# Performance work log

Measured on AMD Instinct MI355X. Metric: run time of the kernel, lower is better.

## Reference

```python
import jax, jax.numpy as jnp
import numpy as np

SEQ_LEN = 2048
NUM_HEADS = 16
DIM_EMB = 1024
DIM_HEAD = DIM_EMB // NUM_HEADS  # 64
DIM_K = DIM_EMB  # source scales by dim_k**-0.5 with dim_k defaulting to dim_emb
BASE = 10000
EPS = float(np.finfo(np.float32).eps)


def _rope_tables(seq_len, dim_head):
    idx = jnp.arange(seq_len, dtype=jnp.float32)
    scale = 1.0 / (BASE ** (jnp.arange(0, dim_head, 2, dtype=jnp.float32) / dim_head) + EPS)
    pos = jnp.outer(idx, scale)              # [S, dh/2]
    pos = jnp.concatenate([pos, pos], axis=-1)  # [S, dh]
    return jnp.cos(pos), jnp.sin(pos)


def _rotate_half(x):
    x1, x2 = x[..., : DIM_HEAD // 2], x[..., DIM_HEAD // 2 :]
    return jnp.concatenate([-x2, x1], axis=-1)


def _apply_rope(x, cos, sin):
    # x: [B, H, S, dh]; cos/sin: [S, dh]
    return x * cos[None, None] + _rotate_half(x) * sin[None, None]


def setup_inputs() -> dict:
    key = jax.random.key(0)
    k1, k2, k3 = jax.random.split(key, 3)
    x = jax.random.normal(k1, (2, SEQ_LEN, DIM_EMB), dtype=jnp.float32)
    Wqkv = jax.random.normal(k2, (DIM_EMB, 3 * DIM_EMB), dtype=jnp.float32) * 0.02
    Wout = jax.random.normal(k3, (DIM_EMB, DIM_EMB), dtype=jnp.float32) * 0.02
    return {"x": x, "Wqkv": Wqkv, "Wout": Wout}


def reference(x, Wqkv, Wout):
    B = x.shape[0]
    cos, sin = _rope_tables(SEQ_LEN, DIM_HEAD)
    qkv = x @ Wqkv  # [B, S, 3*E]
    q, k, v = jnp.split(qkv, 3, axis=-1)

    def to_heads(t):
        return t.reshape(B, SEQ_LEN, NUM_HEADS, DIM_HEAD).transpose(0, 2, 1, 3)

    q, k, v = to_heads(q), to_heads(k), to_heads(v)
    q = _apply_rope(q, cos, sin)
    k = _apply_rope(k, cos, sin)

    scores = jnp.einsum('bhsd,bhtd->bhst', q, k) * (DIM_K ** -0.5)
    causal_mask = jnp.triu(jnp.ones((SEQ_LEN, SEQ_LEN), dtype=bool), k=1)
    scores = jnp.where(causal_mask[None, None], -jnp.inf, scores)
    attn = jax.nn.softmax(scores, axis=-1)
    out = jnp.einsum('bhst,bhtd->bhsd', attn, v)
    out = out.transpose(0, 2, 1, 3).reshape(B, SEQ_LEN, DIM_EMB)
    return out @ Wout
```

## Files before the change

### kernel.cpp

```cpp
#include <hip/hip_runtime.h>

#define S_LEN 2048
#define NHEAD 16

using f32x4  = __attribute__((ext_vector_type(4))) float;
using f32x16 = __attribute__((ext_vector_type(16))) float;
using bf16x8 = __attribute__((ext_vector_type(8))) __bf16;

__device__ __forceinline__ unsigned short f2bf(float f) {
  union { float f; unsigned u; } v; v.f = f;
  unsigned r = v.u + 0x7FFFu + ((v.u >> 16) & 1u);
  return (unsigned short)(r >> 16);
}
__device__ __forceinline__ float bf2f(unsigned short h) {
  union { unsigned u; float f; } v; v.u = ((unsigned)h) << 16; return v.f;
}
__device__ __forceinline__ void unpack8(uint4 u, float x[8]) {
  x[0]=bf2f((unsigned short)(u.x&0xffff)); x[1]=bf2f((unsigned short)(u.x>>16));
  x[2]=bf2f((unsigned short)(u.y&0xffff)); x[3]=bf2f((unsigned short)(u.y>>16));
  x[4]=bf2f((unsigned short)(u.z&0xffff)); x[5]=bf2f((unsigned short)(u.z>>16));
  x[6]=bf2f((unsigned short)(u.w&0xffff)); x[7]=bf2f((unsigned short)(u.w>>16));
}
__device__ __forceinline__ uint4 pack8(const unsigned short o[8]) {
  uint4 u;
  u.x = (unsigned)o[0] | ((unsigned)o[1]<<16);
  u.y = (unsigned)o[2] | ((unsigned)o[3]<<16);
  u.z = (unsigned)o[4] | ((unsigned)o[5]<<16);
  u.w = (unsigned)o[6] | ((unsigned)o[7]<<16);
  return u;
}
__device__ __forceinline__ void gload16(const void* g, void* l) {
  __builtin_amdgcn_global_load_lds(
      (const __attribute__((address_space(1))) unsigned int*)g,
      (__attribute__((address_space(3))) unsigned int*)l, 16, 0, 0);
}
__device__ __forceinline__ float exp2_fast(float x) {
#if __has_builtin(__builtin_amdgcn_exp2f)
  return __builtin_amdgcn_exp2f(x);
#else
  return __expf(x * 0.6931471805599453f);
#endif
}
__device__ __forceinline__ void store_c(float* C, size_t off, float v) { C[off] = v; }
__device__ __forceinline__ void store_c(unsigned short* C, size_t off, float v) { C[off] = f2bf(v); }

__global__ __launch_bounds__(256) void k_cvt(const float* __restrict__ in,
                                             unsigned short* __restrict__ out, int n8) {
  int i = blockIdx.x * 256 + threadIdx.x;
  if (i >= n8) return;
  const float4* p = (const float4*)in + 2 * (size_t)i;
  float4 a = p[0], b = p[1];
  unsigned short o[8] = { f2bf(a.x), f2bf(a.y), f2bf(a.z), f2bf(a.w),
                          f2bf(b.x), f2bf(b.y), f2bf(b.z), f2bf(b.w) };
  ((uint4*)out)[i] = pack8(o);
}

__global__ __launch_bounds__(256) void k_transpose_cvt(const float* __restrict__ in,
                                                       unsigned short* __restrict__ out,
                                                       int R, int C) {
  __shared__ float T[64][65];
  int r0 = blockIdx.x * 64, c0 = blockIdx.y * 64;
  int tid = threadIdx.x;
#pragma unroll
  for (int i = 0; i < 16; ++i) {
    int idx = tid + i * 256;
    int r = idx >> 6, c = idx & 63;
    T[r][c] = in[(size_t)(r0 + r) * C + c0 + c];
  }
  __syncthreads();
#pragma unroll
  for (int i = 0; i < 8; ++i) {
    int idx = tid + i * 256;
    int co = idx >> 5, rp = (idx & 31) * 2;
    unsigned v = (unsigned)f2bf(T[rp][co]) | ((unsigned)f2bf(T[rp + 1][co]) << 16);
    *(unsigned*)&out[(size_t)(c0 + co) * R + r0 + rp] = v;
  }
}

template <typename OUT_T>
__global__ __launch_bounds__(256) void k_gemm_bt(const unsigned short* __restrict__ A,
                                                 const unsigned short* __restrict__ Bt,
                                                 OUT_T* __restrict__ C,
                                                 int M, int N, int K) {
  __shared__ unsigned short As[128 * 32];
  __shared__ unsigned short Bs[128 * 32];
  int m0 = blockIdx.x * 128, n0 = blockIdx.y * 128;
  int tid = threadIdx.x;
  int lane = tid & 63, w = tid >> 6;
  int wr = w >> 1, wc = w & 1;
  int li = lane & 15, g = lane >> 4;

  const unsigned short* a_s0 = A + (size_t)(m0 + (tid >> 2)) * K + (tid & 3) * 8;
  const unsigned short* a_s1 = A + (size_t)(m0 + 64 + (tid >> 2)) * K + (tid & 3) * 8;
  const unsigned short* b_s0 = Bt + (size_t)(n0 + (tid >> 2)) * K + (tid & 3) * 8;
  const unsigned short* b_s1 = Bt + (size_t)(n0 + 64 + (tid >> 2)) * K + (tid & 3) * 8;
  unsigned short* As_d0 = &As[(w * 64) * 8];
  unsigned short* As_d1 = &As[(256 + w * 64) * 8];
  unsigned short* Bs_d0 = &Bs[(w * 64) * 8];
  unsigned short* Bs_d1 = &Bs[(256 + w * 64) * 8];

  f32x4 acc[4][4];
#pragma unroll
  for (int i = 0; i < 4; ++i)
#pragma unroll
    for (int j = 0; j < 4; ++j) acc[i][j] = (f32x4){0.f, 0.f, 0.f, 0.f};

  int nk = K >> 5;
  for (int kt = 0; kt < nk; ++kt) {
    int k0 = kt << 5;
    gload16(a_s0 + k0, As_d0);
    gload16(a_s1 + k0, As_d1);
    gload16(b_s0 + k0, Bs_d0);
    gload16(b_s1 + k0, Bs_d1);
    __syncthreads();
    bf16x8 af[4], bfr[4];
#pragma unroll
    for (int i = 0; i < 4; ++i)
      af[i] = *(const bf16x8*)&As[(wr * 64 + i * 16 + li) * 32 + g * 8];
#pragma unroll
    for (int j = 0; j < 4; ++j)
      bfr[j] = *(const bf16x8*)&Bs[(wc * 64 + j * 16 + li) * 32 + g * 8];
#pragma unroll
    for (int i = 0; i < 4; ++i)
#pragma unroll
      for (int j = 0; j < 4; ++j)
        acc[i][j] = __builtin_amdgcn_mfma_f32_16x16x32_bf16(af[i], bfr[j], acc[i][j], 0, 0, 0);
    __syncthreads();
  }
#pragma unroll
  for (int i = 0; i < 4; ++i) {
    int row = m0 + wr * 64 + i * 16 + g * 4;
#pragma unroll
    for (int j = 0; j < 4; ++j) {
      int col = n0 + wc * 64 + j * 16 + li;
#pragma unroll
      for (int r = 0; r < 4; ++r) store_c(C, (size_t)(row + r) * N + col, acc[i][j][r]);
    }
  }
}

__global__ __launch_bounds__(512, 2) void k_gemm8(const unsigned short* __restrict__ A,
                                                  const unsigned short* __restrict__ Bt,
                                                  unsigned short* __restrict__ C,
                                                  int M, int N, int K) {
  __shared__ unsigned short As[2][256][64];
  __shared__ unsigned short Bs[2][256][64];
  const int tid = threadIdx.x;
  const int lane = tid & 63, w = tid >> 6;
  const int wm = w >> 2, wn = w & 3;
  const int li = lane & 15, g = lane >> 4;
  const int m0 = blockIdx.x * 256, n0 = blockIdx.y * 256;
  const int srow = w * 8 + (lane >> 3);
  const int scol = ((lane & 7) ^ ((lane >> 3) & 7)) * 8;

  f32x4 acc[8][4];
#pragma unroll
  for (int i = 0; i < 8; ++i)
#pragma unroll
    for (int j = 0; j < 4; ++j) acc[i][j] = (f32x4){0.f, 0.f, 0.f, 0.f};

  const int nt = K >> 6;

  auto stage_tile = [&](int kt) {
    int buf = kt & 1;
    const unsigned short* sa = A + (size_t)(m0 + srow) * K + kt * 64 + scol;
    const unsigned short* sb = Bt + (size_t)(n0 + srow) * K + kt * 64 + scol;
    char* da = (char*)&As[buf][0][0] + w * 1024;
    char* db = (char*)&Bs[buf][0][0] + w * 1024;
    gload16(sa, da);
    gload16(sa + (size_t)64 * K, da + 8192);
    gload16(sa + (size_t)128 * K, da + 16384);
    gload16(sa + (size_t)192 * K, da + 24576);
    gload16(sb, db);
    gload16(sb + (size_t)64 * K, db + 8192);
    gload16(sb + (size_t)128 * K, db + 16384);
    gload16(sb + (size_t)192 * K, db + 24576);
  };

  stage_tile(0);

  for (int i = 0; i < nt; ++i) {
    if (i + 1 < nt) {
      stage_tile(i + 1);
      asm volatile("s_waitcnt vmcnt(8)" ::: "memory");
    } else {
      asm volatile("s_waitcnt vmcnt(0)" ::: "memory");
    }
    __builtin_amdgcn_s_barrier();
    asm volatile("" ::: "memory");
    const int buf = i & 1;
#pragma unroll
    for (int kk = 0; kk < 2; ++kk) {
      bf16x8 af[8], bfv[4];
      const int ps = ((kk << 2) | g) ^ (li & 7);
#pragma unroll
      for (int ii = 0; ii < 8; ++ii)
        af[ii] = *(const bf16x8*)&As[buf][wm * 128 + ii * 16 + li][ps * 8];
#pragma unroll
      for (int jj = 0; jj < 4; ++jj)
        bfv[jj] = *(const bf16x8*)&Bs[buf][wn * 64 + jj * 16 + li][ps * 8];
      __builtin_amdgcn_s_setprio(1);
#pragma unroll
      for (int ii = 0; ii < 8; ++ii)
#pragma unroll
        for (int jj = 0; jj < 4; ++jj)
          acc[ii][jj] = __builtin_amdgcn_mfma_f32_16x16x32_bf16(af[ii], bfv[jj],
                                                                acc[ii][jj], 0, 0, 0);
      __builtin_amdgcn_s_setprio(0);
    }
    asm volatile("" ::: "memory");
    __builtin_amdgcn_s_barrier();
    asm volatile("" ::: "memory");
  }

#pragma unroll
  for (int ii = 0; ii < 8; ++ii) {
    int row = m0 + wm * 128 + ii * 16 + g * 4;
#pragma unroll
    for (int jj = 0; jj < 4; ++jj) {
      int col = n0 + wn * 64 + jj * 16 + li;
#pragma unroll
      for (int r = 0; r < 4; ++r) C[(size_t)(row + r) * N + col] = f2bf(acc[ii][jj][r]);
    }
  }
}

__global__ __launch_bounds__(256) void k_rope_split(const unsigned short* __restrict__ qkv,
                                                    unsigned short* __restrict__ Qf,
                                                    unsigned short* __restrict__ Kf,
                                                    unsigned short* __restrict__ Vf) {
  int blk = blockIdx.x;
  int st = blk & 31, h = (blk >> 5) & 15, b = blk >> 9;
  int s0 = st * 64;
  int tid = threadIdx.x;
  int sl = tid >> 2, quad = tid & 3;
  int s = s0 + sl;
  int bh = b * NHEAD + h;
  int l31 = s & 31;
  int qt = s >> 5;
  int cq = quad >> 1, hiq = quad & 1;

  float cs[8], sn[8];
#pragma unroll
  for (int j = 0; j < 8; ++j) {
    int pr = quad * 8 + j;
    float e2 = exp2_fast((float)pr * 0.41524101f);
    float freq = 1.0f / (e2 + 1.1920928955078125e-07f);
    float x = (float)s * freq * 0.15915494309189535f;
    x -= floorf(x);
    float ang = x * 6.283185307179586f;
    sn[j] = __sinf(ang);
    cs[j] = __cosf(ang);
  }
  const unsigned short* row = qkv + (size_t)(b * S_LEN + s) * 3072;
  const float QSC = 0.04508422f;
  {
    float x1[8], x2[8];
    unpack8(*(const uint4*)&row[h * 64 + quad * 8], x1);
    unpack8(*(const uint4*)&row[h * 64 + 32 + quad * 8], x2);
    unsigned short o1[8], o2[8];
#pragma unroll
    for (int j = 0; j < 8; ++j) {
      o1[j] = f2bf((x1[j] * cs[j] - x2[j] * sn[j]) * QSC);
      o2[j] = f2bf((x2[j] * cs[j] + x1[j] * sn[j]) * QSC);
    }
    size_t base = ((size_t)bh * 64 + qt) * 4;
    int lane8 = (hiq * 32 + l31) * 8;
    *(uint4*)&Qf[(base + cq) * 512 + lane8] = pack8(o1);
    *(uint4*)&Qf[(base + 2 + cq) * 512 + lane8] = pack8(o2);
  }
  {
    float x1[8], x2[8];
    unpack8(*(const uint4*)&row[1024 + h * 64 + quad * 8], x1);
    unpack8(*(const uint4*)&row[1024 + h * 64 + 32 + quad * 8], x2);
    unsigned short o1[8], o2[8];
#pragma unroll
    for (int j = 0; j < 8; ++j) {
      o1[j] = f2bf(x1[j] * cs[j] - x2[j] * sn[j]);
      o2[j] = f2bf(x2[j] * cs[j] + x1[j] * sn[j]);
    }
    int lp = (l31 & 0x13) | ((l31 & 4) << 1) | ((l31 & 8) >> 1);
    size_t base = ((size_t)bh * 64 + qt) * 4;
    int lane8 = (hiq * 32 + lp) * 8;
    *(uint4*)&Kf[(base + cq) * 512 + lane8] = pack8(o1);
    *(uint4*)&Kf[(base + 2 + cq) * 512 + lane8] = pack8(o2);
  }
  __shared__ unsigned short Vl[64 * 72];
#pragma unroll
  for (int i = 0; i < 2; ++i) {
    int c = tid + i * 256;
    int r = c >> 3, c8 = (c & 7) * 8;
    *(uint4*)&Vl[r * 72 + c8] =
        *(const uint4*)&qkv[(size_t)(b * S_LEN + s0 + r) * 3072 + 2048 + h * 64 + c8];
  }
  __syncthreads();
  int d = tid >> 2, sc4 = tid & 3;
  unsigned o[8];
#pragma unroll
  for (int jj = 0; jj < 8; ++jj) {
    int sidx = sc4 * 16 + jj * 2;
    o[jj] = (unsigned)Vl[sidx * 72 + d] | ((unsigned)Vl[(sidx + 1) * 72 + d] << 16);
  }
  {
    int t = st * 2 + (sc4 >> 1);
    int c = ((d >> 5) << 1) + (sc4 & 1);
    size_t base = (((size_t)bh * 64 + t) * 4 + c) * 512;
    *(uint4*)&Vf[base + (d & 31) * 8]        = make_uint4(o[0], o[1], o[2], o[3]);
    *(uint4*)&Vf[base + (32 + (d & 31)) * 8] = make_uint4(o[4], o[5], o[6], o[7]);
  }
}

__global__ __launch_bounds__(256) void k_attn4(const unsigned short* __restrict__ Qf,
                                               const unsigned short* __restrict__ Kf,
                                               const unsigned short* __restrict__ Vf,
                                               unsigned short* __restrict__ O) {
  __shared__ float MBUF[3][2176];
  int bid = blockIdx.x;
  int i = (bid & 7) * 256 + (bid >> 3);
  int bh = i >> 6;
  int qt = 63 - (i & 63);
  int tid = threadIdx.x, w = tid >> 6, lane = tid & 63;
  int b = bh >> 4, h = bh & 15;
  int l31 = lane & 31, hi = lane >> 5;

  int n = qt + 1;
  int t0 = (w * n) >> 2, t1 = ((w + 1) * n) >> 2;

  const unsigned short* Kg = Kf + ((size_t)bh * 64) * 4 * 512 + lane * 8;
  const unsigned short* Vg = Vf + ((size_t)bh * 64) * 4 * 512 + lane * 8;

  float m_run = -1e30f, l_run = 0.f;
  f32x16 acc0, acc1;
#pragma unroll
  for (int r = 0; r < 16; ++r) { acc0[r] = 0.f; acc1[r] = 0.f; }

  if (t0 < t1) {
    const unsigned short* Qg = Qf + (((size_t)bh * 64 + qt) * 4) * 512 + lane * 8;
    bf16x8 qf[4];
#pragma unroll
    for (int c = 0; c < 4; ++c) qf[c] = *(const bf16x8*)(Qg + c * 512);

    auto loadK = [&](bf16x8 (&kf)[4], int t) {
      const unsigned short* kp = Kg + (size_t)t * 2048;
#pragma unroll
      for (int c = 0; c < 4; ++c) kf[c] = *(const bf16x8*)(kp + c * 512);
    };
    auto loadV = [&](bf16x8 (&vf)[4], int t) {
      const unsigned short* vp = Vg + (size_t)t * 2048;
#pragma unroll
      for (int c = 0; c < 4; ++c) vf[c] = *(const bf16x8*)(vp + c * 512);
    };
    auto step = [&](bf16x8 (&kf)[4], bf16x8 (&vf)[4], int t) {
      f32x16 s;
#pragma unroll
      for (int r = 0; r < 16; ++r) s[r] = 0.f;
      __builtin_amdgcn_s_setprio(1);
      s = __builtin_amdgcn_mfma_f32_32x32x16_bf16(kf[0], qf[0], s, 0, 0, 0);
      s = __builtin_amdgcn_mfma_f32_32x32x16_bf16(kf[1], qf[1], s, 0, 0, 0);
      s = __builtin_amdgcn_mfma_f32_32x32x16_bf16(kf[2], qf[2], s, 0, 0, 0);
      s = __builtin_amdgcn_mfma_f32_32x32x16_bf16(kf[3], qf[3], s, 0, 0, 0);
      __builtin_amdgcn_s_setprio(0);
      if (t == qt) {
#pragma unroll
        for (int r = 0; r < 16; ++r) {
          int kv = (r & 7) + 16 * (r >> 3) + 8 * hi;
          if (kv > l31) s[r] = -1e30f;
        }
      }
      float pmax;
      {
        float m0 = fmaxf(s[0], s[1]),   mm1 = fmaxf(s[2], s[3]);
        float m2 = fmaxf(s[4], s[5]),   m3 = fmaxf(s[6], s[7]);
        float m4 = fmaxf(s[8], s[9]),   m5 = fmaxf(s[10], s[11]);
        float m6 = fmaxf(s[12], s[13]), m7 = fmaxf(s[14], s[15]);
        m0 = fmaxf(m0, mm1); m2 = fmaxf(m2, m3); m4 = fmaxf(m4, m5); m6 = fmaxf(m6, m7);
        pmax = fmaxf(fmaxf(m0, m2), fmaxf(m4, m6));
      }
      if (__any(pmax > m_run + 8.0f)) {
        float pfull = fmaxf(pmax, __shfl_xor(pmax, 32));
        float mnew = fmaxf(m_run, pfull);
        float fac = exp2_fast(m_run - mnew);
        l_run *= fac;
#pragma unroll
        for (int r = 0; r < 16; ++r) { acc0[r] *= fac; acc1[r] *= fac; }
        m_run = mnew;
      }
#pragma unroll
      for (int r = 0; r < 16; ++r) s[r] = exp2_fast(s[r] - m_run);
      {
        float s0 = (s[0] + s[1]) + (s[2] + s[3]);
        float s1 = (s[4] + s[5]) + (s[6] + s[7]);
        float s2 = (s[8] + s[9]) + (s[10] + s[11]);
        float s3 = (s[12] + s[13]) + (s[14] + s[15]);
        l_run += (s0 + s1) + (s2 + s3);
      }
      bf16x8 pf0, pf1;
      {
        unsigned w0, w1, w2, w3;
        asm("v_cvt_pk_bf16_f32 %0, %1, %2" : "=v"(w0) : "v"(s[0]), "v"(s[1]));
        asm("v_cvt_pk_bf16_f32 %0, %1, %2" : "=v"(w1) : "v"(s[2]), "v"(s[3]));
        asm("v_cvt_pk_bf16_f32 %0, %1, %2" : "=v"(w2) : "v"(s[4]), "v"(s[5]));
        asm("v_cvt_pk_bf16_f32 %0, %1, %2" : "=v"(w3) : "v"(s[6]), "v"(s[7]));
        union { uint4 uu; bf16x8 v; } cv;
        cv.uu = make_uint4(w0, w1, w2, w3);
        pf0 = cv.v;
        asm("v_cvt_pk_bf16_f32 %0, %1, %2" : "=v"(w0) : "v"(s[8]), "v"(s[9]));
        asm("v_cvt_pk_bf16_f32 %0, %1, %2" : "=v"(w1) : "v"(s[10]), "v"(s[11]));
        asm("v_cvt_pk_bf16_f32 %0, %1, %2" : "=v"(w2) : "v"(s[12]), "v"(s[13]));
        asm("v_cvt_pk_bf16_f32 %0, %1, %2" : "=v"(w3) : "v"(s[14]), "v"(s[15]));
        cv.uu = make_uint4(w0, w1, w2, w3);
        pf1 = cv.v;
      }
      __builtin_amdgcn_s_setprio(1);
      acc0 = __builtin_amdgcn_mfma_f32_32x32x16_bf16(vf[0], pf0, acc0, 0, 0, 0);
      acc0 = __builtin_amdgcn_mfma_f32_32x32x16_bf16(vf[1], pf1, acc0, 0, 0, 0);
      acc1 = __builtin_amdgcn_mfma_f32_32x32x16_bf16(vf[2], pf0, acc1, 0, 0, 0);
      acc1 = __builtin_amdgcn_mfma_f32_32x32x16_bf16(vf[3], pf1, acc1, 0, 0, 0);
      __builtin_amdgcn_s_setprio(0);
    };

    bf16x8 kA[4], vA[4], kB[4], vB[4];
    loadK(kA, t0); loadV(vA, t0);
    int t = t0;
    while (true) {
      if (t + 1 < t1) { loadK(kB, t + 1); loadV(vB, t + 1); }
      step(kA, vA, t);
      ++t; if (t >= t1) break;
      if (t + 1 < t1) { loadK(kA, t + 1); loadV(vA, t + 1); }
      step(kB, vB, t);
      ++t; if (t >= t1) break;
    }
  }

  if (w != 0) {
    float* sb = &MBUF[w - 1][0];
#pragma unroll
    for (int r = 0; r < 16; ++r) {
      sb[r * 64 + lane] = acc0[r];
      sb[(16 + r) * 64 + lane] = acc1[r];
    }
    sb[2048 + lane] = m_run;
    sb[2112 + lane] = l_run;
  }
  __syncthreads();
  if (w == 0) {
    float m1 = MBUF[0][2048 + lane], m2 = MBUF[1][2048 + lane], m3 = MBUF[2][2048 + lane];
    float mF = fmaxf(fmaxf(m_run, m1), fmaxf(m2, m3));
    float f0 = exp2_fast(m_run - mF);
    float f1 = exp2_fast(m1 - mF);
    float f2 = exp2_fast(m2 - mF);
    float f3 = exp2_fast(m3 - mF);
    float lF = f0 * l_run + f1 * MBUF[0][2112 + lane] + f2 * MBUF[1][2112 + lane] +
               f3 * MBUF[2][2112 + lane];
    lF += __shfl_xor(lF, 32);
    float inv = 1.0f / lF;
    f32x16 o0, o1;
#pragma unroll
    for (int r = 0; r < 16; ++r) {
      o0[r] = (f0 * acc0[r] + f1 * MBUF[0][r * 64 + lane] + f2 * MBUF[1][r * 64 + lane] +
               f3 * MBUF[2][r * 64 + lane]) * inv;
      o1[r] = (f0 * acc1[r] + f1 * MBUF[0][(16 + r) * 64 + lane] +
               f2 * MBUF[1][(16 + r) * 64 + lane] + f3 * MBUF[2][(16 + r) * 64 + lane]) * inv;
    }
    unsigned short* ol = (unsigned short*)&MBUF[0][0];
#pragma unroll
    for (int dh = 0; dh < 2; ++dh) {
#pragma unroll
      for (int r = 0; r < 16; r += 2) {
        int dv = dh * 32 + (r & 3) + 8 * (r >> 2) + 4 * hi;
        float lo = dh ? o1[r] : o0[r];
        float hi_ = dh ? o1[r + 1] : o0[r + 1];
        unsigned uu;
        asm("v_cvt_pk_bf16_f32 %0, %1, %2" : "=v"(uu) : "v"(lo), "v"(hi_));
        *(unsigned*)&ol[l31 * 72 + dv] = uu;
      }
    }
    asm volatile("s_waitcnt lgkmcnt(0)" ::: "memory");
    int q0f = qt * 32;
    int q = lane >> 1, half = lane & 1;
    unsigned short* op = O + ((size_t)(b * S_LEN + q0f + q)) * 1024 + h * 64 + half * 32;
#pragma unroll
    for (int j = 0; j < 4; ++j)
      *(uint4*)(op + j * 8) = *(const uint4*)&ol[q * 72 + half * 32 + j * 8];
  }
}

extern "C" void kernel_launch(void* const* d_in, const int* in_sizes, int n_in,
                              void* d_out, int out_size, void* d_ws, size_t ws_size,
                              hipStream_t stream) {
  const float* x = (const float*)d_in[0];
  const float* Wqkv = (const float*)d_in[1];
  const float* Wout = (const float*)d_in[2];
  float* out = (float*)d_out;
  char* ws = (char*)d_ws;
  unsigned short* xb = (unsigned short*)(ws);
  unsigned short* WqkvT = (unsigned short*)(ws + ((size_t)8 << 20));
  unsigned short* WoutT = (unsigned short*)(ws + ((size_t)14 << 20));
  unsigned short* qkv = (unsigned short*)(ws + ((size_t)16 << 20));
  unsigned short* Qf = (unsigned short*)(ws + ((size_t)40 << 20));
  unsigned short* Kf = (unsigned short*)(ws + ((size_t)48 << 20));
  unsigned short* Vf = (unsigned short*)(ws + ((size_t)56 << 20));

  k_cvt<<<2048, 256, 0, stream>>>(x, xb, 4096 * 1024 / 8);
  k_transpose_cvt<<<dim3(16, 48), 256, 0, stream>>>(Wqkv, WqkvT, 1024, 3072);
  k_transpose_cvt<<<dim3(16, 16), 256, 0, stream>>>(Wout, WoutT, 1024, 1024);
  k_gemm8<<<dim3(16, 12), 512, 0, stream>>>(xb, WqkvT, qkv, 4096, 3072, 1024);
  k_rope_split<<<1024, 256, 0, stream>>>(qkv, Qf, Kf, Vf);
  k_attn4<<<2048, 256, 0, stream>>>(Qf, Kf, Vf, xb );
  k_gemm_bt<float><<<dim3(32, 8), 256, 0, stream>>>(xb, WoutT, out, 4096, 1024, 1024);
}
```

Before: 128.7 us.

## Unify both projection GEMMs into a double-buffered 128x128 swizzled kernel

Replaces the 256x256-tile QKV GEMM and the simple single-buffered output GEMM with one templated 128x128-tile kernel. It uses double-buffered LDS with an XOR swizzle and a K-step of 64. The QKV projection now launches 768 blocks instead of 192, which fills the 256 CUs better. The output projection gets prefetching and bank-conflict-free LDS reads. In exchange, each block reuses less data per tile, so global and LDS traffic per FLOP goes up.

```diff
diff --git a/kernel.cpp b/kernel.cpp
--- a/kernel.cpp
+++ b/kernel.cpp
@@ -78,84 +78,23 @@
 }
 
 template <typename OUT_T>
-__global__ __launch_bounds__(256) void k_gemm_bt(const unsigned short* __restrict__ A,
-                                                 const unsigned short* __restrict__ Bt,
-                                                 OUT_T* __restrict__ C,
-                                                 int M, int N, int K) {
-  __shared__ unsigned short As[128 * 32];
-  __shared__ unsigned short Bs[128 * 32];
-  int m0 = blockIdx.x * 128, n0 = blockIdx.y * 128;
-  int tid = threadIdx.x;
-  int lane = tid & 63, w = tid >> 6;
-  int wr = w >> 1, wc = w & 1;
-  int li = lane & 15, g = lane >> 4;
-
-  const unsigned short* a_s0 = A + (size_t)(m0 + (tid >> 2)) * K + (tid & 3) * 8;
-  const unsigned short* a_s1 = A + (size_t)(m0 + 64 + (tid >> 2)) * K + (tid & 3) * 8;
-  const unsigned short* b_s0 = Bt + (size_t)(n0 + (tid >> 2)) * K + (tid & 3) * 8;
-  const unsigned short* b_s1 = Bt + (size_t)(n0 + 64 + (tid >> 2)) * K + (tid & 3) * 8;
-  unsigned short* As_d0 = &As[(w * 64) * 8];
-  unsigned short* As_d1 = &As[(256 + w * 64) * 8];
-  unsigned short* Bs_d0 = &Bs[(w * 64) * 8];
-  unsigned short* Bs_d1 = &Bs[(256 + w * 64) * 8];
-
-  f32x4 acc[4][4];
-#pragma unroll
-  for (int i = 0; i < 4; ++i)
-#pragma unroll
-    for (int j = 0; j < 4; ++j) acc[i][j] = (f32x4){0.f, 0.f, 0.f, 0.f};
-
-  int nk = K >> 5;
-  for (int kt = 0; kt < nk; ++kt) {
-    int k0 = kt << 5;
-    gload16(a_s0 + k0, As_d0);
-    gload16(a_s1 + k0, As_d1);
-    gload16(b_s0 + k0, Bs_d0);
-    gload16(b_s1 + k0, Bs_d1);
-    __syncthreads();
-    bf16x8 af[4], bfr[4];
-#pragma unroll
-    for (int i = 0; i < 4; ++i)
-      af[i] = *(const bf16x8*)&As[(wr * 64 + i * 16 + li) * 32 + g * 8];
-#pragma unroll
-    for (int j = 0; j < 4; ++j)
-      bfr[j] = *(const bf16x8*)&Bs[(wc * 64 + j * 16 + li) * 32 + g * 8];
-#pragma unroll
-    for (int i = 0; i < 4; ++i)
-#pragma unroll
-      for (int j = 0; j < 4; ++j)
-        acc[i][j] = __builtin_amdgcn_mfma_f32_16x16x32_bf16(af[i], bfr[j], acc[i][j], 0, 0, 0);
-    __syncthreads();
-  }
-#pragma unroll
-  for (int i = 0; i < 4; ++i) {
-    int row = m0 + wr * 64 + i * 16 + g * 4;
-#pragma unroll
-    for (int j = 0; j < 4; ++j) {
-      int col = n0 + wc * 64 + j * 16 + li;
-#pragma unroll
-      for (int r = 0; r < 4; ++r) store_c(C, (size_t)(row + r) * N + col, acc[i][j][r]);
-    }
-  }
-}
-
-__global__ __launch_bounds__(512, 2) void k_gemm8(const unsigned short* __restrict__ A,
-                                                  const unsigned short* __restrict__ Bt,
-                                                  unsigned short* __restrict__ C,
-                                                  int M, int N, int K) {
-  __shared__ unsigned short As[2][256][64];
-  __shared__ unsigned short Bs[2][256][64];
+__global__ __launch_bounds__(256, 2) void k_gemm128(const unsigned short* __restrict__ A,
+                                                    const unsigned short* __restrict__ Bt,
+                                                    OUT_T* __restrict__ C,
+                                                    int M, int N, int K) {
+  __shared__ unsigned short As[2][128][64];
+  __shared__ unsigned short Bs[2][128][64];
   const int tid = threadIdx.x;
   const int lane = tid & 63, w = tid >> 6;
-  const int wm = w >> 2, wn = w & 3;
+  const int wm = w >> 1, wn = w & 1;
   const int li = lane & 15, g = lane >> 4;
-  const int m0 = blockIdx.x * 256, n0 = blockIdx.y * 256;
+  const int m0 = blockIdx.x * 128, n0 = blockIdx.y * 128;
   const int srow = w * 8 + (lane >> 3);
   const int scol = ((lane & 7) ^ ((lane >> 3) & 7)) * 8;
 
-  f32x4 acc[8][4];
-#pragma unroll
-  for (int i = 0; i < 8; ++i)
+  f32x4 acc[4][4];
+#pragma unroll
+  for (int i = 0; i < 4; ++i)
 #pragma unroll
     for (int j = 0; j < 4; ++j) acc[i][j] = (f32x4){0.f, 0.f, 0.f, 0.f};
 
@@ -165,16 +104,13 @@
     int buf = kt & 1;
     const unsigned short* sa = A + (size_t)(m0 + srow) * K + kt * 64 + scol;
     const unsigned short* sb = Bt + (size_t)(n0 + srow) * K + kt * 64 + scol;
-    char* da = (char*)&As[buf][0][0] + w * 1024;
-    char* db = (char*)&Bs[buf][0][0] + w * 1024;
-    gload16(sa, da);
-    gload16(sa + (size_t)64 * K, da + 8192);
-    gload16(sa + (size_t)128 * K, da + 16384);
-    gload16(sa + (size_t)192 * K, da + 24576);
-    gload16(sb, db);
-    gload16(sb + (size_t)64 * K, db + 8192);
-    gload16(sb + (size_t)128 * K, db + 16384);
-    gload16(sb + (size_t)192 * K, db + 24576);
+    char* da = (char*)&As[buf][srow][0];
+    char* db = (char*)&Bs[buf][srow][0];
+#pragma unroll
+    for (int j = 0; j < 4; ++j) {
+      gload16(sa + (size_t)(j * 32) * K, da + j * 32 * 128);
+      gload16(sb + (size_t)(j * 32) * K, db + j * 32 * 128);
+    }
   };
 
   stage_tile(0);
@@ -191,17 +127,17 @@
     const int buf = i & 1;
 #pragma unroll
     for (int kk = 0; kk < 2; ++kk) {
-      bf16x8 af[8], bfv[4];
+      bf16x8 af[4], bfv[4];
       const int ps = ((kk << 2) | g) ^ (li & 7);
 #pragma unroll
-      for (int ii = 0; ii < 8; ++ii)
-        af[ii] = *(const bf16x8*)&As[buf][wm * 128 + ii * 16 + li][ps * 8];
+      for (int ii = 0; ii < 4; ++ii)
+        af[ii] = *(const bf16x8*)&As[buf][wm * 64 + ii * 16 + li][ps * 8];
 #pragma unroll
       for (int jj = 0; jj < 4; ++jj)
         bfv[jj] = *(const bf16x8*)&Bs[buf][wn * 64 + jj * 16 + li][ps * 8];
       __builtin_amdgcn_s_setprio(1);
 #pragma unroll
-      for (int ii = 0; ii < 8; ++ii)
+      for (int ii = 0; ii < 4; ++ii)
 #pragma unroll
         for (int jj = 0; jj < 4; ++jj)
           acc[ii][jj] = __builtin_amdgcn_mfma_f32_16x16x32_bf16(af[ii], bfv[jj],
@@ -214,13 +150,13 @@
   }
 
 #pragma unroll
-  for (int ii = 0; ii < 8; ++ii) {
-    int row = m0 + wm * 128 + ii * 16 + g * 4;
+  for (int ii = 0; ii < 4; ++ii) {
+    int row = m0 + wm * 64 + ii * 16 + g * 4;
 #pragma unroll
     for (int jj = 0; jj < 4; ++jj) {
       int col = n0 + wn * 64 + jj * 16 + li;
 #pragma unroll
-      for (int r = 0; r < 4; ++r) C[(size_t)(row + r) * N + col] = f2bf(acc[ii][jj][r]);
+      for (int r = 0; r < 4; ++r) store_c(C, (size_t)(row + r) * N + col, acc[ii][jj][r]);
     }
   }
 }
@@ -504,8 +440,8 @@
   k_cvt<<<2048, 256, 0, stream>>>(x, xb, 4096 * 1024 / 8);
   k_transpose_cvt<<<dim3(16, 48), 256, 0, stream>>>(Wqkv, WqkvT, 1024, 3072);
   k_transpose_cvt<<<dim3(16, 16), 256, 0, stream>>>(Wout, WoutT, 1024, 1024);
-  k_gemm8<<<dim3(16, 12), 512, 0, stream>>>(xb, WqkvT, qkv, 4096, 3072, 1024);
+  k_gemm128<unsigned short><<<dim3(32, 24), 256, 0, stream>>>(xb, WqkvT, qkv, 4096, 3072, 1024);
   k_rope_split<<<1024, 256, 0, stream>>>(qkv, Qf, Kf, Vf);
   k_attn4<<<2048, 256, 0, stream>>>(Qf, Kf, Vf, xb );
-  k_gemm_bt<float><<<dim3(32, 8), 256, 0, stream>>>(xb, WoutT, out, 4096, 1024, 1024);
-}
+  k_gemm128<float><<<dim3(32, 8), 256, 0, stream>>>(xb, WoutT, out, 4096, 1024, 1024);
+}
```

Measured after the change: 121.9 us. -5.3%, faster.
